# Performance work log

Hardware: AMD Instinct MI355X
Metric: run time of the kernel (lower is better)

## Reference

```python
import jax, jax.numpy as jnp
import numpy as np

B, S, DIM_IN, DIM_K, DIM_V = 4, 2048, 512, 2048, 64


def setup_inputs() -> dict:
    key = jax.random.key(0)
    k1, k2, k3, k4 = jax.random.split(key, 4)
    x = jax.random.normal(k1, (B, S, DIM_IN), dtype=jnp.float32)
    # nn.Linear(dim_in, d, bias=False) -> stored transposed here so y = x @ W
    Wq = jax.random.normal(k2, (DIM_IN, DIM_K), dtype=jnp.float32) / np.sqrt(DIM_IN)
    Wk = jax.random.normal(k3, (DIM_IN, DIM_K), dtype=jnp.float32) / np.sqrt(DIM_IN)
    Wv = jax.random.normal(k4, (DIM_IN, DIM_V), dtype=jnp.float32) / np.sqrt(DIM_IN)
    return {"x": x, "Wq": Wq, "Wk": Wk, "Wv": Wv}


def reference(x, Wq, Wk, Wv):
    dim_k = Wq.shape[-1]
    q = x @ Wq            # [B, S, dim_k]
    k = x @ Wk            # [B, S, dim_k]
    v = x @ Wv            # [B, S, dim_v]
    scores = jnp.einsum("bqd,bkd->bqk", q, k)  # [B, S, S]
    # causal mask: disallow attending to strictly-future positions
    seq = scores.shape[-1]
    mask = jnp.triu(jnp.ones((seq, seq), dtype=bool), k=1)
    scores = jnp.where(mask[None, :, :], -jnp.inf, scores)
    attn = jax.nn.softmax(scores / np.sqrt(dim_k).astype(np.float32), axis=-1)
    return attn @ v       # [B, S, dim_v]
```

## Files before the change

### kernel.cpp

```cpp
#include <hip/hip_runtime.h>
#include <hip/hip_bf16.h>
#include <math.h>

using bf16 = __hip_bfloat16;
typedef __bf16 bf16x8 __attribute__((ext_vector_type(8)));
typedef float floatx4 __attribute__((ext_vector_type(4)));

constexpr int BB = 4, SS = 2048, DIN = 512, DKK = 2048, DVV = 64;
constexpr int ROWS = BB * SS;
constexpr int LDY = 640;

constexpr size_t XB_OFF  = 0;
constexpr size_t WQB_OFF = XB_OFF  + 8388608;
constexpr size_t WKB_OFF = WQB_OFF + 2097152;
constexpr size_t WT2_OFF = WKB_OFF + 2097152;
constexpr size_t MTP_OFF = WT2_OFF + 655360;
constexpr size_t YV_OFF  = MTP_OFF + 8388608;
constexpr size_t VT_OFF  = YV_OFF  + 10485760;
constexpr size_t PRT_OFF = VT_OFF  + 1048576;
constexpr size_t STA_OFF = PRT_OFF + 16777216;

__device__ __forceinline__ void async_copy16(const bf16* g, const unsigned short* l) {
    __builtin_amdgcn_global_load_lds((const __attribute__((address_space(1))) void*)g,
                                     (__attribute__((address_space(3))) void*)l, 16, 0, 0);
}

__global__ __launch_bounds__(256) void prep(const float* __restrict__ x,
                                            const float* __restrict__ Wq,
                                            const float* __restrict__ Wk,
                                            const float* __restrict__ Wv,
                                            bf16* __restrict__ xb,
                                            bf16* __restrict__ wqb,
                                            bf16* __restrict__ wkb,
                                            bf16* __restrict__ wt2) {
    __shared__ float tile[32][33];
    const int bid = blockIdx.x;
    const int tid = threadIdx.x;

    if (bid < 4096) {
        int i = bid * 256 + tid;
        float4 v = reinterpret_cast<const float4*>(x)[i];
        union { bf16 h[4]; ushort4 u; } cv;
        cv.h[0] = __float2bfloat16(v.x);
        cv.h[1] = __float2bfloat16(v.y);
        cv.h[2] = __float2bfloat16(v.z);
        cv.h[3] = __float2bfloat16(v.w);
        reinterpret_cast<ushort4*>(xb)[i] = cv.u;
    } else if (bid < 6144) {
        int i = (bid - 4096) * 256 + tid;
        const float* src = (i < 262144) ? Wq : Wk;
        bf16* dst = (i < 262144) ? wqb : wkb;
        int j = (i < 262144) ? i : i - 262144;
        float4 v = reinterpret_cast<const float4*>(src)[j];
        union { bf16 h[4]; ushort4 u; } cv;
        cv.h[0] = __float2bfloat16(v.x);
        cv.h[1] = __float2bfloat16(v.y);
        cv.h[2] = __float2bfloat16(v.z);
        cv.h[3] = __float2bfloat16(v.w);
        reinterpret_cast<ushort4*>(dst)[j] = cv.u;
    } else {
        int idx = bid - 6144;
        int n0 = (idx & 1) * 32;
        int k0 = (idx >> 1) * 32;
        int nn = tid & 31, kk8 = tid >> 5;
        #pragma unroll
        for (int p = 0; p < 4; ++p) {
            int k = p * 8 + kk8;
            tile[k][nn] = Wv[(long long)(k0 + k) * 64 + n0 + nn];
        }
        __syncthreads();
        int kk = tid & 31, nn8 = tid >> 5;
        #pragma unroll
        for (int p = 0; p < 4; ++p) {
            int n = p * 8 + nn8;
            wt2[(long long)(512 + n0 + n) * 512 + k0 + kk] = __float2bfloat16(tile[kk][n]);
        }
    }
}

__global__ __launch_bounds__(256) void gemm_mt(const bf16* __restrict__ A,
                                               const bf16* __restrict__ Bt,
                                               float* __restrict__ Cp) {
    __shared__ __align__(16) unsigned short As[64 * 64];
    __shared__ __align__(16) unsigned short Bs[64 * 64];

    const int tid = threadIdx.x;
    const int lane = tid & 63, wave = tid >> 6;

    const int wg = (blockIdx.x & 7) * 64 + (blockIdx.x >> 3);
    const int z = wg >> 6;
    const int tile = wg & 63;
    const long long m0 = (long long)(tile >> 3) * 64;
    const long long n0 = (long long)(tile & 7) * 64;
    const int koff = z * 256;

    const int rIn = lane >> 3;
    const int cSwz = ((lane & 7) ^ rIn) * 8;
    const int wm0 = (wave >> 1) * 32, wn0 = (wave & 1) * 32;
    const int l15 = lane & 15, quad = lane >> 4;
    const int sw7 = l15 & 7;

    floatx4 acc[2][2] = {};

    for (int k0 = koff; k0 < koff + 256; k0 += 64) {
        #pragma unroll
        for (int t0 = 0; t0 < 4; ++t0) {
            int t = t0 * 4 + wave;
            if (t < 8)
                async_copy16(A + (m0 + t * 8 + rIn) * 2048LL + k0 + cSwz, &As[t * 512]);
            else
                async_copy16(Bt + (n0 + (t - 8) * 8 + rIn) * 2048LL + k0 + cSwz, &Bs[(t - 8) * 512]);
        }
        __syncthreads();
        #pragma unroll
        for (int sk = 0; sk < 2; ++sk) {
            const int rchunk = (((sk << 2) | quad) ^ sw7) * 8;
            bf16x8 af[2], bfr[2];
            #pragma unroll
            for (int mi = 0; mi < 2; ++mi)
                af[mi] = *reinterpret_cast<const bf16x8*>(&As[(wm0 + mi * 16 + l15) * 64 + rchunk]);
            #pragma unroll
            for (int ni = 0; ni < 2; ++ni)
                bfr[ni] = *reinterpret_cast<const bf16x8*>(&Bs[(wn0 + ni * 16 + l15) * 64 + rchunk]);
            #pragma unroll
            for (int mi = 0; mi < 2; ++mi)
                #pragma unroll
                for (int ni = 0; ni < 2; ++ni)
                    acc[mi][ni] = __builtin_amdgcn_mfma_f32_16x16x32_bf16(af[mi], bfr[ni],
                                                                          acc[mi][ni], 0, 0, 0);
        }
        __syncthreads();
    }

    float* C = Cp + (long long)z * 262144;
    #pragma unroll
    for (int mi = 0; mi < 2; ++mi) {
        long long row0 = m0 + wm0 + mi * 16 + quad * 4;
        #pragma unroll
        for (int ni = 0; ni < 2; ++ni) {
            long long col = n0 + wn0 + ni * 16 + l15;
            #pragma unroll
            for (int r = 0; r < 4; ++r)
                C[(row0 + r) * 512 + col] = acc[mi][ni][r];
        }
    }
}

__global__ __launch_bounds__(256) void reduce_mt(const float4* __restrict__ part,
                                                 bf16* __restrict__ wt2) {
    int i = blockIdx.x * 256 + threadIdx.x;
    float4 s = {0.f, 0.f, 0.f, 0.f};
    #pragma unroll
    for (int t = 0; t < 8; ++t) {
        float4 a = part[(long long)t * 65536 + i];
        s.x += a.x; s.y += a.y; s.z += a.z; s.w += a.w;
    }
    union { bf16 h[4]; ushort4 u; } cv;
    cv.h[0] = __float2bfloat16(s.x);
    cv.h[1] = __float2bfloat16(s.y);
    cv.h[2] = __float2bfloat16(s.z);
    cv.h[3] = __float2bfloat16(s.w);
    reinterpret_cast<ushort4*>(wt2)[i] = cv.u;
}

__global__ __launch_bounds__(256) void gemm_proj(const bf16* __restrict__ A,
                                                 const bf16* __restrict__ Bt,
                                                 bf16* __restrict__ C,
                                                 bf16* __restrict__ vt) {
    __shared__ __align__(16) unsigned short As[8 * 512];
    __shared__ __align__(16) unsigned short Bs[16 * 512];

    const int tid = threadIdx.x;
    const int lane = tid & 63, wave = tid >> 6;

    const int wg = (blockIdx.x & 7) * 80 + (blockIdx.x >> 3);
    const long long m0 = (long long)(wg / 5) * 64;
    const int ntile = wg % 5;
    const long long n0 = (long long)ntile * 128;

    const int rIn = lane >> 3;
    const int cSwz = ((lane & 7) ^ rIn) * 8;
    const int wm0 = (wave >> 1) * 32, wn0 = (wave & 1) * 64;
    const int l15 = lane & 15, quad = lane >> 4;
    const int sw7 = l15 & 7;

    floatx4 acc[2][4] = {};

    for (int k0 = 0; k0 < DIN; k0 += 64) {
        #pragma unroll
        for (int t0 = 0; t0 < 6; ++t0) {
            int t = t0 * 4 + wave;
            if (t < 8)
                async_copy16(A + (m0 + t * 8 + rIn) * (long long)DIN + k0 + cSwz, &As[t * 512]);
            else
                async_copy16(Bt + (n0 + (t - 8) * 8 + rIn) * (long long)DIN + k0 + cSwz,
                             &Bs[(t - 8) * 512]);
        }
        __syncthreads();
        #pragma unroll
        for (int sk = 0; sk < 2; ++sk) {
            const int rchunk = (((sk << 2) | quad) ^ sw7) * 8;
            bf16x8 af[2], bfr[4];
            #pragma unroll
            for (int mi = 0; mi < 2; ++mi)
                af[mi] = *reinterpret_cast<const bf16x8*>(&As[(wm0 + mi * 16 + l15) * 64 + rchunk]);
            #pragma unroll
            for (int ni = 0; ni < 4; ++ni)
                bfr[ni] = *reinterpret_cast<const bf16x8*>(&Bs[(wn0 + ni * 16 + l15) * 64 + rchunk]);
            #pragma unroll
            for (int mi = 0; mi < 2; ++mi)
                #pragma unroll
                for (int ni = 0; ni < 4; ++ni)
                    acc[mi][ni] = __builtin_amdgcn_mfma_f32_16x16x32_bf16(af[mi], bfr[ni],
                                                                          acc[mi][ni], 0, 0, 0);
        }
        __syncthreads();
    }

    if (ntile < 4) {
        #pragma unroll
        for (int mi = 0; mi < 2; ++mi) {
            long long row0 = m0 + wm0 + mi * 16 + quad * 4;
            #pragma unroll
            for (int ni = 0; ni < 4; ++ni) {
                long long col = n0 + wn0 + ni * 16 + l15;
                #pragma unroll
                for (int r = 0; r < 4; ++r)
                    C[(row0 + r) * (long long)LDY + col] = __float2bfloat16(acc[mi][ni][r]);
            }
        }
    } else if (!(wave & 1)) {
        const int b = (int)(m0 >> 11);
        const int sbase = ((int)m0 & 2047) + wm0;
        #pragma unroll
        for (int mi = 0; mi < 2; ++mi) {
            int s0 = sbase + mi * 16 + quad * 4;
            #pragma unroll
            for (int ni = 0; ni < 4; ++ni) {
                int j = ni * 16 + l15;
                union { bf16 h[4]; ushort4 u; } cv;
                #pragma unroll
                for (int r = 0; r < 4; ++r)
                    cv.h[r] = __float2bfloat16(acc[mi][ni][r]);
                *reinterpret_cast<ushort4*>(vt + ((long long)(b * DVV + j)) * SS + s0) = cv.u;
            }
        }
    }
}

__global__ __launch_bounds__(256) void attn_fused(const bf16* __restrict__ yv,
                                                  const bf16* __restrict__ xb,
                                                  const bf16* __restrict__ vt,
                                                  bf16* __restrict__ part,
                                                  float* __restrict__ stats) {
    constexpr int BK = 64;
    constexpr float SCALE = 0.022097086912079608f;

    __shared__ __align__(16) char smem[24576];
    unsigned short* As = (unsigned short*)smem;
    unsigned short* Bs = (unsigned short*)(smem + 8192);
    unsigned short* Ps = (unsigned short*)smem;
    unsigned short* Vs = (unsigned short*)(smem + 9216);
    float* smax = (float*)(smem + 18432);
    float* ssum = (float*)(smem + 18944);

    const int wg = (blockIdx.x & 7) * 34 + (blockIdx.x >> 3);
    int by = 0, c = 0;
    while (c + (by >> 1) + 1 <= wg) { c += (by >> 1) + 1; ++by; }
    const int bx = wg - c;
    const int b = blockIdx.z;

    const bf16* A  = yv + (long long)b * SS * LDY;
    const bf16* Bt = xb + (long long)b * SS * 512;

    const int tid = threadIdx.x;
    const int lane = tid & 63, wave = tid >> 6;
    const long long m0 = (long long)by * 64;
    const long long n0 = (long long)bx * 128;

    const int rIn = lane >> 3;
    const int cSwz = ((lane & 7) ^ rIn) * 8;
    const int wm0 = (wave >> 1) * 32, wn0 = (wave & 1) * 64;
    const int l15 = lane & 15, quad = lane >> 4;
    const int sw7 = l15 & 7;

    floatx4 acc[2][4] = {};

    uint4 vreg[4];
    {
        int j = tid >> 2;
        int ch = tid & 3;
        #pragma unroll
        for (int p = 0; p < 4; ++p)
            vreg[p] = *reinterpret_cast<const uint4*>(
                vt + ((long long)b * DVV + j) * SS + n0 + (ch + p * 4) * 8);
    }

    auto issue = [&](int k0) {
        #pragma unroll
        for (int t0 = 0; t0 < 6; ++t0) {
            int t = t0 * 4 + wave;
            if (t < 8)
                async_copy16(A + (m0 + t * 8 + rIn) * (long long)LDY + k0 + cSwz,
                             &As[t * 512]);
            else
                async_copy16(Bt + (n0 + (t - 8) * 8 + rIn) * 512LL + k0 + cSwz,
                             &Bs[(t - 8) * 512]);
        }
    };

    for (int it = 0; it < DIN / BK; ++it) {
        issue(it * BK);
        __syncthreads();
        __builtin_amdgcn_s_setprio(1);
        #pragma unroll
        for (int sk = 0; sk < 2; ++sk) {
            const int rchunk = (((sk << 2) | quad) ^ sw7) * 8;
            bf16x8 af[2], bfr[4];
            #pragma unroll
            for (int mi = 0; mi < 2; ++mi)
                af[mi] = *reinterpret_cast<const bf16x8*>(
                    &As[(wm0 + mi * 16 + l15) * BK + rchunk]);
            #pragma unroll
            for (int ni = 0; ni < 4; ++ni)
                bfr[ni] = *reinterpret_cast<const bf16x8*>(
                    &Bs[(wn0 + ni * 16 + l15) * BK + rchunk]);
            #pragma unroll
            for (int mi = 0; mi < 2; ++mi)
                #pragma unroll
                for (int ni = 0; ni < 4; ++ni)
                    acc[mi][ni] = __builtin_amdgcn_mfma_f32_16x16x32_bf16(af[mi], bfr[ni],
                                                                          acc[mi][ni], 0, 0, 0);
        }
        __builtin_amdgcn_s_setprio(0);
        __syncthreads();
    }

    const bool diag = (n0 + 127 > m0);
    #pragma unroll
    for (int mi = 0; mi < 2; ++mi)
        #pragma unroll
        for (int ni = 0; ni < 4; ++ni)
            #pragma unroll
            for (int r = 0; r < 4; ++r) {
                float v = acc[mi][ni][r] * SCALE;
                if (diag) {
                    int grow = (int)m0 + wm0 + mi * 16 + quad * 4 + r;
                    int gcol = (int)n0 + wn0 + ni * 16 + l15;
                    if (gcol > grow) v = -INFINITY;
                }
                acc[mi][ni][r] = v;
            }

    float rmax[2][4];
    #pragma unroll
    for (int mi = 0; mi < 2; ++mi)
        #pragma unroll
        for (int r = 0; r < 4; ++r) {
            float m = fmaxf(fmaxf(acc[mi][0][r], acc[mi][1][r]),
                            fmaxf(acc[mi][2][r], acc[mi][3][r]));
            #pragma unroll
            for (int msk = 8; msk >= 1; msk >>= 1) m = fmaxf(m, __shfl_xor(m, msk));
            rmax[mi][r] = m;
            if (l15 == 0) smax[(wm0 + mi * 16 + quad * 4 + r) * 2 + (wave & 1)] = m;
        }
    __syncthreads();
    #pragma unroll
    for (int mi = 0; mi < 2; ++mi)
        #pragma unroll
        for (int r = 0; r < 4; ++r) {
            int row = wm0 + mi * 16 + quad * 4 + r;
            rmax[mi][r] = fmaxf(smax[row * 2], smax[row * 2 + 1]);
        }

    #pragma unroll
    for (int mi = 0; mi < 2; ++mi)
        #pragma unroll
        for (int r = 0; r < 4; ++r) {
            float s = 0.f;
            #pragma unroll
            for (int ni = 0; ni < 4; ++ni) {
                float p = __expf(acc[mi][ni][r] - rmax[mi][r]);
                acc[mi][ni][r] = p;
                s += p;
            }
            #pragma unroll
            for (int msk = 8; msk >= 1; msk >>= 1) s += __shfl_xor(s, msk);
            if (l15 == 0) ssum[(wm0 + mi * 16 + quad * 4 + r) * 2 + (wave & 1)] = s;
        }

    if ((wave & 1) == 0) {
        #pragma unroll
        for (int mi = 0; mi < 2; ++mi) {
            int row = wm0 + mi * 16 + quad * 4;
            #pragma unroll
            for (int ni = 0; ni < 4; ++ni) {
                int col = ni * 16 + l15;
                #pragma unroll
                for (int r = 0; r < 4; ++r)
                    Ps[(row + r) * 72 + col] =
                        (unsigned short)__bfloat16_as_ushort(__float2bfloat16(acc[mi][ni][r]));
            }
        }
    }
    {
        int j = tid >> 2;
        int ch = tid & 3;
        #pragma unroll
        for (int pp = 0; pp < 2; ++pp) {
            int chh = ch + pp * 4;
            *reinterpret_cast<uint4*>(&Vs[j * 72 + ((chh ^ (j & 7)) * 8)]) = vreg[pp];
        }
    }
    __syncthreads();

    if (tid < 64) {
        float m = fmaxf(smax[tid * 2], smax[tid * 2 + 1]);
        float l = ssum[tid * 2] + ssum[tid * 2 + 1];
        long long o = (((long long)b * 16 + bx) * SS + m0 + tid) * 2;
        stats[o] = m;
        stats[o + 1] = l;
    }

    const int wmv = wave * 16;
    floatx4 accO[4] = {};
    __builtin_amdgcn_s_setprio(1);
    #pragma unroll
    for (int sk = 0; sk < 2; ++sk) {
        bf16x8 af = *reinterpret_cast<const bf16x8*>(
            &Ps[(wmv + l15) * 72 + sk * 32 + quad * 8]);
        #pragma unroll
        for (int ni = 0; ni < 4; ++ni) {
            bf16x8 bfv = *reinterpret_cast<const bf16x8*>(
                &Vs[(ni * 16 + l15) * 72 + ((((sk << 2) | quad)) ^ sw7) * 8]);
            accO[ni] = __builtin_amdgcn_mfma_f32_16x16x32_bf16(af, bfv, accO[ni], 0, 0, 0);
        }
    }
    __builtin_amdgcn_s_setprio(0);
    __syncthreads();

    if ((wave & 1) == 1) {
        #pragma unroll
        for (int mi = 0; mi < 2; ++mi) {
            int row = wm0 + mi * 16 + quad * 4;
            #pragma unroll
            for (int ni = 0; ni < 4; ++ni) {
                int col = ni * 16 + l15;
                #pragma unroll
                for (int r = 0; r < 4; ++r)
                    Ps[(row + r) * 72 + col] =
                        (unsigned short)__bfloat16_as_ushort(__float2bfloat16(acc[mi][ni][r]));
            }
        }
    }
    {
        int j = tid >> 2;
        int ch = tid & 3;
        #pragma unroll
        for (int pp = 0; pp < 2; ++pp) {
            int chh = ch + pp * 4;
            *reinterpret_cast<uint4*>(&Vs[j * 72 + ((chh ^ (j & 7)) * 8)]) = vreg[2 + pp];
        }
    }
    __syncthreads();

    __builtin_amdgcn_s_setprio(1);
    #pragma unroll
    for (int sk = 0; sk < 2; ++sk) {
        bf16x8 af = *reinterpret_cast<const bf16x8*>(
            &Ps[(wmv + l15) * 72 + sk * 32 + quad * 8]);
        #pragma unroll
        for (int ni = 0; ni < 4; ++ni) {
            bf16x8 bfv = *reinterpret_cast<const bf16x8*>(
                &Vs[(ni * 16 + l15) * 72 + ((((sk << 2) | quad)) ^ sw7) * 8]);
            accO[ni] = __builtin_amdgcn_mfma_f32_16x16x32_bf16(af, bfv, accO[ni], 0, 0, 0);
        }
    }
    __builtin_amdgcn_s_setprio(0);

    #pragma unroll
    for (int ni = 0; ni < 4; ++ni)
        #pragma unroll
        for (int r = 0; r < 4; ++r)
            part[(((long long)b * 16 + bx) * SS + m0 + wmv + quad * 4 + r) * 64 + ni * 16 + l15]
                = __float2bfloat16(accO[ni][r]);
}

__global__ __launch_bounds__(256) void combine(const bf16* __restrict__ part,
                                               const float* __restrict__ stats,
                                               float* __restrict__ out) {
    int tid = blockIdx.x * 256 + threadIdx.x;
    int row = tid >> 3;
    int col8 = (tid & 7) * 8;
    int b = row >> 11, s = row & (SS - 1);
    int nt = (s >> 7) + 1;

    float m[16], l[16], M = -INFINITY;
    #pragma unroll
    for (int t = 0; t < 16; ++t)
        if (t < nt) {
            long long o = (((long long)b * 16 + t) * SS + s) * 2;
            m[t] = stats[o];
            l[t] = stats[o + 1];
            M = fmaxf(M, m[t]);
        }
    float O[8] = {};
    float L = 0.f;
    #pragma unroll
    for (int t = 0; t < 16; ++t)
        if (t < nt) {
            float wgt = __expf(m[t] - M);
            L += wgt * l[t];
            union { uint4 q; unsigned short u[8]; } ld;
            ld.q = *reinterpret_cast<const uint4*>(
                part + (((long long)b * 16 + t) * SS + s) * 64 + col8);
            #pragma unroll
            for (int j = 0; j < 8; ++j)
                O[j] += wgt * __uint_as_float((unsigned)ld.u[j] << 16);
        }
    float rinv = 1.0f / L;
    float4 o0 = {O[0] * rinv, O[1] * rinv, O[2] * rinv, O[3] * rinv};
    float4 o1 = {O[4] * rinv, O[5] * rinv, O[6] * rinv, O[7] * rinv};
    float4* dst = reinterpret_cast<float4*>(out + (long long)row * 64 + col8);
    dst[0] = o0;
    dst[1] = o1;
}

extern "C" void kernel_launch(void* const* d_in, const int* in_sizes, int n_in,
                              void* d_out, int out_size, void* d_ws, size_t ws_size,
                              hipStream_t stream) {
    const float* x  = (const float*)d_in[0];
    const float* Wq = (const float*)d_in[1];
    const float* Wk = (const float*)d_in[2];
    const float* Wv = (const float*)d_in[3];
    float* out = (float*)d_out;

    char* w = (char*)d_ws;
    bf16* xb   = (bf16*)(w + XB_OFF);
    bf16* wqb  = (bf16*)(w + WQB_OFF);
    bf16* wkb  = (bf16*)(w + WKB_OFF);
    bf16* wt2  = (bf16*)(w + WT2_OFF);
    float* mtp = (float*)(w + MTP_OFF);
    bf16* yv   = (bf16*)(w + YV_OFF);
    bf16* vt   = (bf16*)(w + VT_OFF);
    bf16* part = (bf16*)(w + PRT_OFF);
    float* stats = (float*)(w + STA_OFF);

    prep<<<6176, 256, 0, stream>>>(x, Wq, Wk, Wv, xb, wqb, wkb, wt2);

    gemm_mt<<<512, 256, 0, stream>>>(wkb, wqb, mtp);
    reduce_mt<<<65536 / 256, 256, 0, stream>>>((const float4*)mtp, wt2);

    gemm_proj<<<640, 256, 0, stream>>>(xb, wt2, yv, vt);

    attn_fused<<<dim3(272, 1, BB), 256, 0, stream>>>(yv, xb, vt, part, stats);

    combine<<<ROWS * 8 / 256, 256, 0, stream>>>(part, stats, out);
}
```

Before: 136.6 us.

## Fuse weight bf16 conversion into Wk^T Wq GEMM and widen attention K-tile

Merges the Wq/Wk fp32-to-bf16 conversion into the Wk·Wq product GEMM by loading fp32 directly, converting in registers and storing to swizzled LDS, folded into one prep kernel with the x conversion and Wv transpose. This removes one launch and the round trip of the bf16 weight copies through global memory. Separately, the attention kernel's first GEMM stage doubles its K-tile from 64 to 128 with a new swizzle, halving barrier-separated iterations at the cost of twice the LDS (48KB), which may reduce occupancy.

```diff
diff --git a/kernel.cpp b/kernel.cpp
--- a/kernel.cpp
+++ b/kernel.cpp
@@ -25,20 +25,94 @@
                                      (__attribute__((address_space(3))) void*)l, 16, 0, 0);
 }
 
-__global__ __launch_bounds__(256) void prep(const float* __restrict__ x,
-                                            const float* __restrict__ Wq,
-                                            const float* __restrict__ Wk,
-                                            const float* __restrict__ Wv,
-                                            bf16* __restrict__ xb,
-                                            bf16* __restrict__ wqb,
-                                            bf16* __restrict__ wkb,
-                                            bf16* __restrict__ wt2) {
-    __shared__ float tile[32][33];
+__global__ __launch_bounds__(256) void prep_mt(const float* __restrict__ x,
+                                               const float* __restrict__ Wq,
+                                               const float* __restrict__ Wk,
+                                               const float* __restrict__ Wv,
+                                               bf16* __restrict__ xb,
+                                               bf16* __restrict__ wt2,
+                                               float* __restrict__ Cp) {
+    __shared__ __align__(16) char sm[16384];
     const int bid = blockIdx.x;
     const int tid = threadIdx.x;
 
-    if (bid < 4096) {
-        int i = bid * 256 + tid;
+    if (bid < 512) {
+        unsigned short* As = (unsigned short*)sm;
+        unsigned short* Bs = (unsigned short*)(sm + 8192);
+        const int lane = tid & 63, wave = tid >> 6;
+
+        const int wg = (bid & 7) * 64 + (bid >> 3);
+        const int z = wg >> 6;
+        const int tile = wg & 63;
+        const long long m0 = (long long)(tile >> 3) * 64;
+        const long long n0 = (long long)(tile & 7) * 64;
+        const int koff = z * 256;
+
+        const int rIn = lane >> 3;
+        const int cSwzE = ((lane & 7) ^ rIn) * 8;
+        const int wm0 = (wave >> 1) * 32, wn0 = (wave & 1) * 32;
+        const int l15 = lane & 15, quad = lane >> 4;
+        const int sw7 = l15 & 7;
+
+        floatx4 acc[2][2] = {};
+
+        for (int k0 = koff; k0 < koff + 256; k0 += 64) {
+            #pragma unroll
+            for (int t0 = 0; t0 < 4; ++t0) {
+                int t = t0 * 4 + wave;
+                const float* src = (t < 8)
+                    ? Wk + (m0 + t * 8 + rIn) * 2048LL + k0 + cSwzE
+                    : Wq + (n0 + (t - 8) * 8 + rIn) * 2048LL + k0 + cSwzE;
+                float4 f0 = *reinterpret_cast<const float4*>(src);
+                float4 f1 = *reinterpret_cast<const float4*>(src + 4);
+                union { bf16 h[8]; uint4 u; } cv;
+                cv.h[0] = __float2bfloat16(f0.x);
+                cv.h[1] = __float2bfloat16(f0.y);
+                cv.h[2] = __float2bfloat16(f0.z);
+                cv.h[3] = __float2bfloat16(f0.w);
+                cv.h[4] = __float2bfloat16(f1.x);
+                cv.h[5] = __float2bfloat16(f1.y);
+                cv.h[6] = __float2bfloat16(f1.z);
+                cv.h[7] = __float2bfloat16(f1.w);
+                unsigned short* dst = (t < 8) ? &As[t * 512 + lane * 8]
+                                              : &Bs[(t - 8) * 512 + lane * 8];
+                *reinterpret_cast<uint4*>(dst) = cv.u;
+            }
+            __syncthreads();
+            #pragma unroll
+            for (int sk = 0; sk < 2; ++sk) {
+                const int rchunk = (((sk << 2) | quad) ^ sw7) * 8;
+                bf16x8 af[2], bfr[2];
+                #pragma unroll
+                for (int mi = 0; mi < 2; ++mi)
+                    af[mi] = *reinterpret_cast<const bf16x8*>(&As[(wm0 + mi * 16 + l15) * 64 + rchunk]);
+                #pragma unroll
+                for (int ni = 0; ni < 2; ++ni)
+                    bfr[ni] = *reinterpret_cast<const bf16x8*>(&Bs[(wn0 + ni * 16 + l15) * 64 + rchunk]);
+                #pragma unroll
+                for (int mi = 0; mi < 2; ++mi)
+                    #pragma unroll
+                    for (int ni = 0; ni < 2; ++ni)
+                        acc[mi][ni] = __builtin_amdgcn_mfma_f32_16x16x32_bf16(af[mi], bfr[ni],
+                                                                              acc[mi][ni], 0, 0, 0);
+            }
+            __syncthreads();
+        }
+
+        float* C = Cp + (long long)z * 262144;
+        #pragma unroll
+        for (int mi = 0; mi < 2; ++mi) {
+            long long row0 = m0 + wm0 + mi * 16 + quad * 4;
+            #pragma unroll
+            for (int ni = 0; ni < 2; ++ni) {
+                long long col = n0 + wn0 + ni * 16 + l15;
+                #pragma unroll
+                for (int r = 0; r < 4; ++r)
+                    C[(row0 + r) * 512 + col] = acc[mi][ni][r];
+            }
+        }
+    } else if (bid < 4608) {
+        int i = (bid - 512) * 256 + tid;
         float4 v = reinterpret_cast<const float4*>(x)[i];
         union { bf16 h[4]; ushort4 u; } cv;
         cv.h[0] = __float2bfloat16(v.x);
@@ -46,20 +120,9 @@
         cv.h[2] = __float2bfloat16(v.z);
         cv.h[3] = __float2bfloat16(v.w);
         reinterpret_cast<ushort4*>(xb)[i] = cv.u;
-    } else if (bid < 6144) {
-        int i = (bid - 4096) * 256 + tid;
-        const float* src = (i < 262144) ? Wq : Wk;
-        bf16* dst = (i < 262144) ? wqb : wkb;
-        int j = (i < 262144) ? i : i - 262144;
-        float4 v = reinterpret_cast<const float4*>(src)[j];
-        union { bf16 h[4]; ushort4 u; } cv;
-        cv.h[0] = __float2bfloat16(v.x);
-        cv.h[1] = __float2bfloat16(v.y);
-        cv.h[2] = __float2bfloat16(v.z);
-        cv.h[3] = __float2bfloat16(v.w);
-        reinterpret_cast<ushort4*>(dst)[j] = cv.u;
     } else {
-        int idx = bid - 6144;
+        float (*tile)[33] = (float (*)[33])sm;
+        int idx = bid - 4608;
         int n0 = (idx & 1) * 32;
         int k0 = (idx >> 1) * 32;
         int nn = tid & 31, kk8 = tid >> 5;
@@ -74,74 +137,6 @@
         for (int p = 0; p < 4; ++p) {
             int n = p * 8 + nn8;
             wt2[(long long)(512 + n0 + n) * 512 + k0 + kk] = __float2bfloat16(tile[kk][n]);
-        }
-    }
-}
-
-__global__ __launch_bounds__(256) void gemm_mt(const bf16* __restrict__ A,
-                                               const bf16* __restrict__ Bt,
-                                               float* __restrict__ Cp) {
-    __shared__ __align__(16) unsigned short As[64 * 64];
-    __shared__ __align__(16) unsigned short Bs[64 * 64];
-
-    const int tid = threadIdx.x;
-    const int lane = tid & 63, wave = tid >> 6;
-
-    const int wg = (blockIdx.x & 7) * 64 + (blockIdx.x >> 3);
-    const int z = wg >> 6;
-    const int tile = wg & 63;
-    const long long m0 = (long long)(tile >> 3) * 64;
-    const long long n0 = (long long)(tile & 7) * 64;
-    const int koff = z * 256;
-
-    const int rIn = lane >> 3;
-    const int cSwz = ((lane & 7) ^ rIn) * 8;
-    const int wm0 = (wave >> 1) * 32, wn0 = (wave & 1) * 32;
-    const int l15 = lane & 15, quad = lane >> 4;
-    const int sw7 = l15 & 7;
-
-    floatx4 acc[2][2] = {};
-
-    for (int k0 = koff; k0 < koff + 256; k0 += 64) {
-        #pragma unroll
-        for (int t0 = 0; t0 < 4; ++t0) {
-            int t = t0 * 4 + wave;
-            if (t < 8)
-                async_copy16(A + (m0 + t * 8 + rIn) * 2048LL + k0 + cSwz, &As[t * 512]);
-            else
-                async_copy16(Bt + (n0 + (t - 8) * 8 + rIn) * 2048LL + k0 + cSwz, &Bs[(t - 8) * 512]);
-        }
-        __syncthreads();
-        #pragma unroll
-        for (int sk = 0; sk < 2; ++sk) {
-            const int rchunk = (((sk << 2) | quad) ^ sw7) * 8;
-            bf16x8 af[2], bfr[2];
-            #pragma unroll
-            for (int mi = 0; mi < 2; ++mi)
-                af[mi] = *reinterpret_cast<const bf16x8*>(&As[(wm0 + mi * 16 + l15) * 64 + rchunk]);
-            #pragma unroll
-            for (int ni = 0; ni < 2; ++ni)
-                bfr[ni] = *reinterpret_cast<const bf16x8*>(&Bs[(wn0 + ni * 16 + l15) * 64 + rchunk]);
-            #pragma unroll
-            for (int mi = 0; mi < 2; ++mi)
-                #pragma unroll
-                for (int ni = 0; ni < 2; ++ni)
-                    acc[mi][ni] = __builtin_amdgcn_mfma_f32_16x16x32_bf16(af[mi], bfr[ni],
-                                                                          acc[mi][ni], 0, 0, 0);
-        }
-        __syncthreads();
-    }
-
-    float* C = Cp + (long long)z * 262144;
-    #pragma unroll
-    for (int mi = 0; mi < 2; ++mi) {
-        long long row0 = m0 + wm0 + mi * 16 + quad * 4;
-        #pragma unroll
-        for (int ni = 0; ni < 2; ++ni) {
-            long long col = n0 + wn0 + ni * 16 + l15;
-            #pragma unroll
-            for (int r = 0; r < 4; ++r)
-                C[(row0 + r) * 512 + col] = acc[mi][ni][r];
         }
     }
 }
@@ -253,12 +248,12 @@
                                                   const bf16* __restrict__ vt,
                                                   bf16* __restrict__ part,
                                                   float* __restrict__ stats) {
-    constexpr int BK = 64;
+    constexpr int BK = 128;
     constexpr float SCALE = 0.022097086912079608f;
 
-    __shared__ __align__(16) char smem[24576];
+    __shared__ __align__(16) char smem[49152];
     unsigned short* As = (unsigned short*)smem;
-    unsigned short* Bs = (unsigned short*)(smem + 8192);
+    unsigned short* Bs = (unsigned short*)(smem + 16384);
     unsigned short* Ps = (unsigned short*)smem;
     unsigned short* Vs = (unsigned short*)(smem + 9216);
     float* smax = (float*)(smem + 18432);
@@ -278,8 +273,8 @@
     const long long m0 = (long long)by * 64;
     const long long n0 = (long long)bx * 128;
 
-    const int rIn = lane >> 3;
-    const int cSwz = ((lane & 7) ^ rIn) * 8;
+    const int rIn2 = lane >> 4;
+    const int c16 = lane & 15;
     const int wm0 = (wave >> 1) * 32, wn0 = (wave & 1) * 64;
     const int l15 = lane & 15, quad = lane >> 4;
     const int sw7 = l15 & 7;
@@ -298,14 +293,17 @@
 
     auto issue = [&](int k0) {
         #pragma unroll
-        for (int t0 = 0; t0 < 6; ++t0) {
+        for (int t0 = 0; t0 < 12; ++t0) {
             int t = t0 * 4 + wave;
-            if (t < 8)
-                async_copy16(A + (m0 + t * 8 + rIn) * (long long)LDY + k0 + cSwz,
-                             &As[t * 512]);
-            else
-                async_copy16(Bt + (n0 + (t - 8) * 8 + rIn) * 512LL + k0 + cSwz,
-                             &Bs[(t - 8) * 512]);
+            if (t < 16) {
+                int row = t * 4 + rIn2;
+                int col = (c16 ^ (row & 7)) * 8;
+                async_copy16(A + (m0 + row) * (long long)LDY + k0 + col, &As[t * 512]);
+            } else {
+                int row = (t - 16) * 4 + rIn2;
+                int col = (c16 ^ (row & 7)) * 8;
+                async_copy16(Bt + (n0 + row) * 512LL + k0 + col, &Bs[(t - 16) * 512]);
+            }
         }
     };
 
@@ -314,7 +312,7 @@
         __syncthreads();
         __builtin_amdgcn_s_setprio(1);
         #pragma unroll
-        for (int sk = 0; sk < 2; ++sk) {
+        for (int sk = 0; sk < 4; ++sk) {
             const int rchunk = (((sk << 2) | quad) ^ sw7) * 8;
             bf16x8 af[2], bfr[4];
             #pragma unroll
@@ -537,8 +535,6 @@
 
     char* w = (char*)d_ws;
     bf16* xb   = (bf16*)(w + XB_OFF);
-    bf16* wqb  = (bf16*)(w + WQB_OFF);
-    bf16* wkb  = (bf16*)(w + WKB_OFF);
     bf16* wt2  = (bf16*)(w + WT2_OFF);
     float* mtp = (float*)(w + MTP_OFF);
     bf16* yv   = (bf16*)(w + YV_OFF);
@@ -546,9 +542,8 @@
     bf16* part = (bf16*)(w + PRT_OFF);
     float* stats = (float*)(w + STA_OFF);
 
-    prep<<<6176, 256, 0, stream>>>(x, Wq, Wk, Wv, xb, wqb, wkb, wt2);
-
-    gemm_mt<<<512, 256, 0, stream>>>(wkb, wqb, mtp);
+    prep_mt<<<4640, 256, 0, stream>>>(x, Wq, Wk, Wv, xb, wt2, mtp);
+
     reduce_mt<<<65536 / 256, 256, 0, stream>>>((const float4*)mtp, wt2);
 
     gemm_proj<<<640, 256, 0, stream>>>(xb, wt2, yv, vt);
```

Result: no change. 136.0 us, median of 2 (-0.4%).
